# Optimization experiments

Measured on AMD Instinct MI355X. Metric: run time of the kernel, lower is better.

Reference implementation:

```python
import jax, jax.numpy as jnp
import numpy as np

BATCH = 16384
N = 4096  # transform size, power of 2


def setup_inputs() -> dict:
    key = jax.random.key(0)
    x = jax.random.normal(key, (BATCH, N), dtype=jnp.float32)
    return {"x": x, "n": N}


def reference(x, n):
    """Fast Walsh-Hadamard transform (Sylvester ordering) along the last axis.

    Equivalent to the recursive slice/cat implementation: H_n = H_2 (x) H_{n/2},
    realized as log2(n) in-place butterfly stages. The Python while-loop runs a
    fixed log2(n) times (static), so it is jit-friendly.
    """
    shape = x.shape
    y = x
    h = 1
    while h < n:
        # pair elements i and i+h within blocks of size 2h
        y = y.reshape(shape[:-1] + (n // (2 * h), 2, h))
        a = y[..., 0, :]
        b = y[..., 1, :]
        y = jnp.stack([a + b, a - b], axis=-2)
        h *= 2
    return y.reshape(shape)
```

## Files before the change

kernel.cpp:

```cpp
#include <hip/hip_runtime.h>


#define WHT_N 4096

__global__ __launch_bounds__(64) void fwht4096_kernel(const float* __restrict__ in,
                                                      float* __restrict__ out) {
    __shared__ float lds[WHT_N];

    const int l = threadIdx.x;
    const long long row = blockIdx.x;
    const float* __restrict__ src = in + row * (long long)WHT_N;
    float* __restrict__ dst = out + row * (long long)WHT_N;

    float x[64];

#pragma unroll
    for (int j = 0; j < 16; ++j) {
        const float4 v = *reinterpret_cast<const float4*>(src + 64 * l + 4 * j);
        x[4 * j + 0] = v.x;
        x[4 * j + 1] = v.y;
        x[4 * j + 2] = v.z;
        x[4 * j + 3] = v.w;
    }

#pragma unroll
    for (int s = 0; s < 6; ++s) {
        const int h = 1 << s;
#pragma unroll
        for (int k0 = 0; k0 < 64; k0 += 2 * (1 << s)) {
#pragma unroll
            for (int m = 0; m < (1 << s); ++m) {
                const float a = x[k0 + m];
                const float b = x[k0 + m + h];
                x[k0 + m] = a + b;
                x[k0 + m + h] = a - b;
            }
        }
    }

#pragma unroll
    for (int j = 0; j < 16; ++j) {
        const int a = 64 * l + 4 * (j ^ (l & 7));
        float4 v;
        v.x = x[4 * j + 0];
        v.y = x[4 * j + 1];
        v.z = x[4 * j + 2];
        v.w = x[4 * j + 3];
        *reinterpret_cast<float4*>(&lds[a]) = v;
    }
    __syncthreads();

#pragma unroll
    for (int k = 0; k < 64; ++k) {
        x[k] = lds[64 * k + (l ^ ((k & 7) << 2))];
    }

#pragma unroll
    for (int s = 0; s < 6; ++s) {
        const int h = 1 << s;
#pragma unroll
        for (int k0 = 0; k0 < 64; k0 += 2 * (1 << s)) {
#pragma unroll
            for (int m = 0; m < (1 << s); ++m) {
                const float a = x[k0 + m];
                const float b = x[k0 + m + h];
                x[k0 + m] = a + b;
                x[k0 + m + h] = a - b;
            }
        }
    }

#pragma unroll
    for (int k = 0; k < 64; ++k) {
        dst[l + 64 * k] = x[k];
    }
}

extern "C" void kernel_launch(void* const* d_in, const int* in_sizes, int n_in,
                              void* d_out, int out_size, void* d_ws, size_t ws_size,
                              hipStream_t stream) {
    const float* x = (const float*)d_in[0];
    float* out = (float*)d_out;
    const int rows = in_sizes[0] / WHT_N;

    dim3 grid(rows);
    dim3 block(64);
    fwht4096_kernel<<<grid, block, 0, stream>>>(x, out);
}
```

Measured before the change: 431.5 us.

## Use 256 threads per row with 16 elements each and multi-pass LDS exchanges

```diff
diff --git a/kernel.cpp b/kernel.cpp
--- a/kernel.cpp
+++ b/kernel.cpp
@@ -3,76 +3,94 @@
 
 #define WHT_N 4096
 
-__global__ __launch_bounds__(64) void fwht4096_kernel(const float* __restrict__ in,
-                                                      float* __restrict__ out) {
+#define BFLY(d)                                          \
+    _Pragma("unroll")                                    \
+    for (int r = 0; r < 16; ++r) {                       \
+        if ((r & (d)) == 0) {                            \
+            const float a_ = x[r], b_ = x[r ^ (d)];      \
+            x[r] = a_ + b_;                              \
+            x[r ^ (d)] = a_ - b_;                        \
+        }                                                \
+    }
+
+__global__ __launch_bounds__(256, 4) void fwht4096_kernel(const float* __restrict__ in,
+                                                          float* __restrict__ out) {
     __shared__ float lds[WHT_N];
 
-    const int l = threadIdx.x;
+    const int t = threadIdx.x;
     const long long row = blockIdx.x;
     const float* __restrict__ src = in + row * (long long)WHT_N;
     float* __restrict__ dst = out + row * (long long)WHT_N;
 
-    float x[64];
+    float x[16];
 
 #pragma unroll
-    for (int j = 0; j < 16; ++j) {
-        const float4 v = *reinterpret_cast<const float4*>(src + 64 * l + 4 * j);
-        x[4 * j + 0] = v.x;
-        x[4 * j + 1] = v.y;
-        x[4 * j + 2] = v.z;
-        x[4 * j + 3] = v.w;
+    for (int i = 0; i < 4; ++i) {
+        const float4 v = *reinterpret_cast<const float4*>(src + (i << 10) + (t << 2));
+        x[4 * i + 0] = v.x;
+        x[4 * i + 1] = v.y;
+        x[4 * i + 2] = v.z;
+        x[4 * i + 3] = v.w;
     }
 
+    BFLY(1)
+    BFLY(2)
+
+    const int tb = (t << 2) ^ (((t >> 4) & 7) << 2);
 #pragma unroll
-    for (int s = 0; s < 6; ++s) {
-        const int h = 1 << s;
-#pragma unroll
-        for (int k0 = 0; k0 < 64; k0 += 2 * (1 << s)) {
-#pragma unroll
-            for (int m = 0; m < (1 << s); ++m) {
-                const float a = x[k0 + m];
-                const float b = x[k0 + m + h];
-                x[k0 + m] = a + b;
-                x[k0 + m + h] = a - b;
-            }
-        }
-    }
-
-#pragma unroll
-    for (int j = 0; j < 16; ++j) {
-        const int a = 64 * l + 4 * (j ^ (l & 7));
-        float4 v;
-        v.x = x[4 * j + 0];
-        v.y = x[4 * j + 1];
-        v.z = x[4 * j + 2];
-        v.w = x[4 * j + 3];
-        *reinterpret_cast<float4*>(&lds[a]) = v;
+    for (int i = 0; i < 4; ++i) {
+        const int a = tb ^ (i << 10) ^ (i << 3);
+        *reinterpret_cast<float4*>(&lds[a]) =
+            make_float4(x[4 * i + 0], x[4 * i + 1], x[4 * i + 2], x[4 * i + 3]);
     }
     __syncthreads();
 
+    const int B1 = (((((t >> 2) & 3) << 10) | ((t >> 4) << 6) | (t & 3))) ^
+                   (((((t >> 4) & 7) ^ (((t >> 2) & 3) << 1))) << 2);
 #pragma unroll
-    for (int k = 0; k < 64; ++k) {
-        x[k] = lds[64 * k + (l ^ ((k & 7) << 2))];
+    for (int r = 0; r < 16; ++r) x[r] = lds[B1 ^ (r << 2)];
+
+    BFLY(1)
+    BFLY(2)
+    BFLY(4)
+    BFLY(8)
+
+    __syncthreads();
+#pragma unroll
+    for (int r = 0; r < 16; ++r) lds[B1 ^ (r << 2)] = x[r];
+    __syncthreads();
+
+    const int B2 = (((((t >> 2) & 3) << 10) | ((t >> 4) << 2) | (t & 3))) ^
+                   ((((t >> 2) & 3)) << 3);
+#pragma unroll
+    for (int r = 0; r < 16; ++r) x[r] = lds[B2 ^ ((r << 6) | ((r & 7) << 2))];
+
+    BFLY(1)
+    BFLY(2)
+    BFLY(4)
+    BFLY(8)
+
+    __syncthreads();
+#pragma unroll
+    for (int r = 0; r < 16; ++r) lds[B2 ^ ((r << 6) | ((r & 7) << 2))] = x[r];
+    __syncthreads();
+
+#pragma unroll
+    for (int i = 0; i < 4; ++i) {
+        const float4 v = *reinterpret_cast<const float4*>(&lds[tb ^ (i << 10) ^ (i << 3)]);
+        x[4 * i + 0] = v.x;
+        x[4 * i + 1] = v.y;
+        x[4 * i + 2] = v.z;
+        x[4 * i + 3] = v.w;
     }
 
-#pragma unroll
-    for (int s = 0; s < 6; ++s) {
-        const int h = 1 << s;
-#pragma unroll
-        for (int k0 = 0; k0 < 64; k0 += 2 * (1 << s)) {
-#pragma unroll
-            for (int m = 0; m < (1 << s); ++m) {
-                const float a = x[k0 + m];
-                const float b = x[k0 + m + h];
-                x[k0 + m] = a + b;
-                x[k0 + m + h] = a - b;
-            }
-        }
-    }
+    BFLY(4)
+    BFLY(8)
 
 #pragma unroll
-    for (int k = 0; k < 64; ++k) {
-        dst[l + 64 * k] = x[k];
+    for (int i = 0; i < 4; ++i) {
+        *reinterpret_cast<float4*>(dst + (i << 10) + (t << 2)) =
+            make_float4(x[4 * i + 0], x[4 * i + 1], x[4 * i + 2], x[4 * i + 3]);
     }
 }
 
@@ -83,7 +101,5 @@
     float* out = (float*)d_out;
     const int rows = in_sizes[0] / WHT_N;
 
-    dim3 grid(rows);
-    dim3 block(64);
-    fwht4096_kernel<<<grid, block, 0, stream>>>(x, out);
+    fwht4096_kernel<<<dim3(rows), dim3(256), 0, stream>>>(x, out);
 }
```

Result: no change. 430.1 us (-0.3%).
